# Kernel tuning notes

Hardware: AMD Instinct MI355X
Metric: run time of the kernel (lower is better)

Reference implementation:

```python
import jax, jax.numpy as jnp
import numpy as np

EMBED_DIM = 512
NUM_HEADS = 8
HEAD_DIM = EMBED_DIM // NUM_HEADS
B, N, M = 4, 4096, 4096


def setup_inputs() -> dict:
    key = jax.random.key(0)
    ks = jax.random.split(key, 16)
    s = 0.02
    inp = {
        "query": jax.random.normal(ks[0], (B, N, EMBED_DIM), jnp.float32),
        "key": jax.random.normal(ks[1], (B, M, EMBED_DIM), jnp.float32),
        "value": jax.random.normal(ks[2], (B, M, EMBED_DIM), jnp.float32),
        # Linear weights stored as (in, out) so y = x @ W + b (== torch x @ W.T + b)
        "Wq": jax.random.normal(ks[3], (EMBED_DIM, EMBED_DIM), jnp.float32) * s,
        "bq": jnp.zeros((EMBED_DIM,), jnp.float32),
        "Wk": jax.random.normal(ks[4], (EMBED_DIM, EMBED_DIM), jnp.float32) * s,
        "bk": jnp.zeros((EMBED_DIM,), jnp.float32),
        "Wv": jax.random.normal(ks[5], (EMBED_DIM, EMBED_DIM), jnp.float32) * s,
        "bv": jnp.zeros((EMBED_DIM,), jnp.float32),
        # rank expansion MLP acts per-head on head_dim
        "W1": jax.random.normal(ks[6], (HEAD_DIM, HEAD_DIM * 2), jnp.float32) * s,
        "b1": jnp.zeros((HEAD_DIM * 2,), jnp.float32),
        "W2": jax.random.normal(ks[7], (HEAD_DIM * 2, HEAD_DIM), jnp.float32) * s,
        "b2": jnp.zeros((HEAD_DIM,), jnp.float32),
        "Wo": jax.random.normal(ks[8], (EMBED_DIM, EMBED_DIM), jnp.float32) * s,
        "bo": jnp.zeros((EMBED_DIM,), jnp.float32),
    }
    return inp


def reference(query, key, value, Wq, bq, Wk, bk, Wv, bv, W1, b1, W2, b2, Wo, bo):
    b, n, _ = query.shape
    m = key.shape[1]
    H, D = NUM_HEADS, HEAD_DIM
    # ELU+1 feature maps on projected q, k
    q = jax.nn.elu(query @ Wq + bq) + 1.0           # [B,N,E]
    k = jax.nn.elu(key @ Wk + bk) + 1.0             # [B,M,E]
    v = value @ Wv + bv                              # [B,M,E]
    q = q.reshape(b, n, H, D)
    k = k.reshape(b, m, H, D)
    v = v.reshape(b, m, H, D)
    # rank expansion MLP on keys (per head_dim), exact GELU as nn.GELU default
    k_aug = jax.nn.gelu(k @ W1 + b1, approximate=False) @ W2 + b2
    k_aug = jax.nn.elu(k_aug) + 1.0                  # [B,M,H,D]
    # inputs already fp32 (torch .float() casts are identity here)
    k_scaled = k_aug / m                             # normalize over context len
    kv_context = jnp.einsum('bmhd,bmhe->bhde', k_scaled, v)   # [B,H,D,D]
    out = jnp.einsum('bnhd,bhde->bnhe', q, kv_context)        # [B,N,H,D]
    k_sum = k_scaled.sum(axis=1)                      # [B,H,D]
    denom = jnp.einsum('bnhd,bhd->bnh', q, k_sum)     # [B,N,H]
    out = out / jnp.clip(denom, 1e-6, None)[..., None]
    out = jnp.clip(jnp.nan_to_num(out, nan=0.0, posinf=65000.0, neginf=-65000.0),
                   -65000.0, 65000.0)
    out = out.reshape(b, n, H * D)
    return out @ Wo + bo
```

## Files before the change

kernel.cpp:

```cpp
#include <hip/hip_runtime.h>
#include <hip/hip_bf16.h>
#include <cmath>

#define DEV __device__ __forceinline__

typedef __bf16 bf16x8 __attribute__((ext_vector_type(8)));
typedef float f32x4 __attribute__((ext_vector_type(4)));
typedef unsigned int u32;
typedef unsigned short u16;

#define S_VMCNT(N) asm volatile("s_waitcnt vmcnt(" #N ")" ::: "memory")
#define S_LGKM0    asm volatile("s_waitcnt lgkmcnt(0)" ::: "memory")
#define S_FENCE    asm volatile("" ::: "memory")
#define S_BAR      __builtin_amdgcn_s_barrier()

DEV u16 f2bf(float f) {
  union { float f; u32 u; } v;
  v.f = f;
  u32 u = v.u;
  u += 0x7fffu + ((u >> 16) & 1u);
  return (u16)(u >> 16);
}
DEV u32 pk2(float a, float b) {
  union { __hip_bfloat162 h2; u32 u; } v;
  v.h2 = __float22bfloat162_rn(float2{a, b});
  return v.u;
}

DEV void async16(const void* g, void* l) {
  __builtin_amdgcn_global_load_lds((const __attribute__((address_space(1))) u32*)g,
                                   (__attribute__((address_space(3))) u32*)l, 16, 0, 0);
}

DEV int swz(int row, int kq) { return row * 64 + ((kq * 8) ^ ((row & 7) << 3)); }

struct PArgs {
  const float* wsrc[6];
  u16* wdst[6];
  int K[6];
  int N[6];
  const float* xsrc[3];
  u16* xdst[3];
};
__global__ __launch_bounds__(256)
void prep_all(PArgs a)
{
  __shared__ u16 t[64][72];
  const int tid = threadIdx.x;

  if (blockIdx.y == 3) {
    const int x = blockIdx.x;
    const int m = x >> 6;
    const int kt = ((x >> 3) & 7) * 64, nt = (x & 7) * 64;
    const int K = a.K[m], N = a.N[m];
    if (kt >= K || nt >= N) return;
    const float* src = a.wsrc[m];
    u16* dst = a.wdst[m];
    const int tx = tid & 15, ty = tid >> 4;
#pragma unroll
    for (int rr = 0; rr < 64; rr += 16) {
      const int k = kt + ty + rr;
      float4 v = *(const float4*)(src + (long)k * N + nt + tx * 4);
      t[tx * 4 + 0][ty + rr] = f2bf(v.x);
      t[tx * 4 + 1][ty + rr] = f2bf(v.y);
      t[tx * 4 + 2][ty + rr] = f2bf(v.z);
      t[tx * 4 + 3][ty + rr] = f2bf(v.w);
    }
    __syncthreads();
    if (m < 4) {
      const int ktile = kt >> 6;
#pragma unroll
      for (int it = 0; it < 2; ++it) {
        const int s = tid + it * 256;
        const int r = s >> 3, c = (s & 7) * 8;
        const int n = nt + r;
        const int colblk = n >> 7, cl = n & 127;
        ushort4 u0 = *(ushort4*)&t[r][c];
        ushort4 u1 = *(ushort4*)&t[r][c + 4];
        u16* d = dst + ((long)colblk * 8 + ktile) * 8192 + cl * 64 + (c ^ ((cl & 7) << 3));
        *(ushort4*)d = u0;
        *(ushort4*)(d + 4) = u1;
      }
    } else {
#pragma unroll
      for (int it = 0; it < 2; ++it) {
        const int s = tid + it * 256;
        const int r = s >> 3, c = (s & 7) * 8;
        ushort4 u0 = *(ushort4*)&t[r][c];
        ushort4 u1 = *(ushort4*)&t[r][c + 4];
        *(ushort4*)(dst + (long)(nt + r) * K + kt + c) = u0;
        *(ushort4*)(dst + (long)(nt + r) * K + kt + c + 4) = u1;
      }
    }
  } else {
    if (blockIdx.x >= 256) return;
    const int z = blockIdx.y;
    const float* src = a.xsrc[z];
    u16* dst = a.xdst[z];
    const long r0 = (long)blockIdx.x * 64;
    const int wv = tid >> 6, lane = tid & 63;
    const int row_lo = lane >> 3, kq = lane & 7;
#pragma unroll 4
    for (int it = 0; it < 16; ++it) {
      const int c = it * 4 + wv;
      const int kt = c & 7, row_hi = c >> 3;
      const int row = row_hi * 8 + row_lo;
      const long ng = r0 + row;
      const int rb = (int)(ng >> 7), rl = (int)(ng & 127);
      const float* s = src + ng * 512 + kt * 64 + kq * 8;
      float4 lo = *(const float4*)s, hi = *(const float4*)(s + 4);
      union { u32 q[4]; uint4 v; } pk;
      pk.q[0] = pk2(lo.x, lo.y); pk.q[1] = pk2(lo.z, lo.w);
      pk.q[2] = pk2(hi.x, hi.y); pk.q[3] = pk2(hi.z, hi.w);
      *(uint4*)(dst + ((long)rb * 8 + kt) * 8192 + rl * 64 + ((kq * 8) ^ ((rl & 7) << 3))) = pk.v;
    }
  }
}

__global__ __launch_bounds__(256, 2)
void qkv_gemm(const u16* __restrict__ qbI, const u16* __restrict__ kbI,
              const u16* __restrict__ vbI, const u16* __restrict__ WqP,
              const u16* __restrict__ WkP, const u16* __restrict__ WvP,
              const float* __restrict__ bq, const float* __restrict__ bk,
              const float* __restrict__ bv, const u16* __restrict__ W1T,
              const u16* __restrict__ W2T, const float* __restrict__ b1,
              const float* __restrict__ b2, u16* __restrict__ qact,
              u16* __restrict__ vT, u16* __restrict__ kaT, float invM)
{
  __shared__ __align__(16) u16 SB[32768];

  const int z = blockIdx.z;
  const u16* Ai = z == 0 ? qbI : z == 1 ? kbI : vbI;
  const u16* Bp = z == 0 ? WqP : z == 1 ? WkP : WvP;
  const float* bias = z == 0 ? bq : z == 1 ? bk : bv;

  const int tid = threadIdx.x, wv = tid >> 6, lane = tid & 63;
  const int wr = wv >> 1, wc = wv & 1;
  const int lrow = lane & 15, lq = lane >> 4;
  const long r0 = (long)blockIdx.x * 128;
  const int c0 = blockIdx.y * 128;

  auto stage = [&](int T, u16* buf) {
#pragma unroll
    for (int it = 0; it < 4; ++it) {
      const int sl = it * 256 + wv * 64;
      async16(Ai + ((long)blockIdx.x * 8 + T) * 8192 + (sl + lane) * 8, &buf[sl * 8]);
      async16(Bp + ((long)blockIdx.y * 8 + T) * 8192 + (sl + lane) * 8, &buf[8192 + sl * 8]);
    }
  };

  f32x4 acc[4][4] = {};
  stage(0, SB);
  S_VMCNT(0);
  S_BAR;

#pragma unroll
  for (int t = 0; t < 8; ++t) {
    const int cur = t & 1, nxt = 1 - cur;
    if (t < 7) stage(t + 1, SB + nxt * 16384);
    const u16* Ac = SB + cur * 16384;
    const u16* Bc = Ac + 8192;
#pragma unroll
    for (int subk = 0; subk < 2; ++subk) {
      bf16x8 af[4], bfr[4];
#pragma unroll
      for (int i = 0; i < 4; ++i)
        af[i] = *(const bf16x8*)&Ac[swz(wr * 64 + i * 16 + lrow, subk * 4 + lq)];
#pragma unroll
      for (int j = 0; j < 4; ++j)
        bfr[j] = *(const bf16x8*)&Bc[swz(wc * 64 + j * 16 + lrow, subk * 4 + lq)];
#pragma unroll
      for (int i = 0; i < 4; ++i)
#pragma unroll
        for (int j = 0; j < 4; ++j)
          acc[i][j] = __builtin_amdgcn_mfma_f32_16x16x32_bf16(af[i], bfr[j], acc[i][j], 0, 0, 0);
    }
    S_LGKM0;
    if (t < 7) { S_VMCNT(0); }
    S_BAR;
  }

  if (z == 0) {
    u16* LTq = SB + wv * 4608;
#pragma unroll
    for (int i = 0; i < 4; ++i) {
#pragma unroll
      for (int j = 0; j < 4; ++j) {
        const int col = c0 + wc * 64 + j * 16 + lrow;
        const float bvv = bias[col];
        const int cloc = j * 16 + lrow;
#pragma unroll
        for (int p = 0; p < 4; ++p) {
          float o = acc[i][j][p] + bvv;
          o = (o > 0.f) ? (o + 1.f) : __expf(o);
          LTq[(i * 16 + lq * 4 + p) * 72 + cloc] = f2bf(o);
        }
      }
    }
    __syncthreads();
#pragma unroll
    for (int ps = 0; ps < 8; ++ps) {
      const int rloc = ps * 8 + (lane >> 3);
      const int coff = (lane & 7) * 8;
      uint4 v = *(const uint4*)&LTq[rloc * 72 + coff];
      *(uint4*)(qact + (r0 + wr * 64 + rloc) * 512 + c0 + wc * 64 + coff) = v;
    }
  } else if (z == 2) {
    u16* LTv = SB + wv * 4608;
#pragma unroll
    for (int i = 0; i < 4; ++i) {
#pragma unroll
      for (int j = 0; j < 4; ++j) {
        const int col = c0 + wc * 64 + j * 16 + lrow;
        const float bvv = bias[col];
        ushort4 w;
        w.x = f2bf(acc[i][j][0] + bvv);
        w.y = f2bf(acc[i][j][1] + bvv);
        w.z = f2bf(acc[i][j][2] + bvv);
        w.w = f2bf(acc[i][j][3] + bvv);
        *(ushort4*)&LTv[(j * 16 + lrow) * 72 + i * 16 + lq * 4] = w;
      }
    }
    const int b = (int)(r0 >> 12);
    const int h = (c0 + wc * 64) >> 6;
    const int mg0 = (int)(r0 & 4095) + wr * 64;
    __syncthreads();
#pragma unroll
    for (int ps = 0; ps < 8; ++ps) {
      const int e = ps * 8 + (lane >> 3);
      const int mq = (lane & 7) * 8;
      uint4 v = *(const uint4*)&LTv[e * 72 + mq];
      *(uint4*)(vT + (((long)b * 8 + h) * 64 + e) * 4096 + mg0 + mq) = v;
    }
  } else {
    u16* As_k = SB;
    u16* hid  = SB + 16384;
    const int b   = (int)(r0 >> 12);
    const int m0g = (int)(r0 & 4095);
    const int h0  = c0 >> 6;

    __syncthreads();
#pragma unroll
    for (int i = 0; i < 4; ++i)
#pragma unroll
      for (int j = 0; j < 4; ++j) {
        const int col = c0 + wc * 64 + j * 16 + lrow;
        const float bvv = bias[col];
        const int d = j * 16 + lrow;
#pragma unroll
        for (int p = 0; p < 4; ++p) {
          const int m = wr * 64 + i * 16 + lq * 4 + p;
          float o = acc[i][j][p] + bvv;
          o = (o > 0.f) ? (o + 1.f) : __expf(o);
          As_k[wc * 8192 + m * 64 + ((((d >> 3) ^ (m & 7)) << 3) | (d & 7))] = f2bf(o);
        }
      }
    __syncthreads();

    const int c0m = (wv >> 1) * 64, mh0 = (wv & 1) * 64;
    const int d0  = (wv >> 1) * 32, mh2 = (wv & 1) * 64;

    for (int hh = 0; hh < 2; ++hh) {
      f32x4 acc1[4][4] = {};
#pragma unroll
      for (int kt = 0; kt < 2; ++kt) {
        bf16x8 wa[4], kb[4];
#pragma unroll
        for (int i = 0; i < 4; ++i)
          wa[i] = *(const bf16x8*)(W1T + (c0m + i * 16 + lrow) * 64 + kt * 32 + lq * 8);
#pragma unroll
        for (int j = 0; j < 4; ++j) {
          const int m = mh0 + j * 16 + lrow;
          kb[j] = *(const bf16x8*)&As_k[hh * 8192 + m * 64 + (((kt * 4 + lq) ^ (m & 7)) << 3)];
        }
#pragma unroll
        for (int i = 0; i < 4; ++i)
#pragma unroll
          for (int j = 0; j < 4; ++j)
            acc1[i][j] = __builtin_amdgcn_mfma_f32_16x16x32_bf16(wa[i], kb[j], acc1[i][j], 0, 0, 0);
      }

#pragma unroll
      for (int i = 0; i < 4; ++i) {
        const int cc = c0m + i * 16 + lq * 4;
        float4 bv4 = *(const float4*)(b1 + cc);
#pragma unroll
        for (int j = 0; j < 4; ++j) {
          const int m = mh0 + j * 16 + lrow;
          float x0 = acc1[i][j][0] + bv4.x, x1 = acc1[i][j][1] + bv4.y;
          float x2 = acc1[i][j][2] + bv4.z, x3 = acc1[i][j][3] + bv4.w;
          ushort4 w;
          w.x = f2bf(0.5f * x0 * (1.f + erff(x0 * 0.7071067811865475f)));
          w.y = f2bf(0.5f * x1 * (1.f + erff(x1 * 0.7071067811865475f)));
          w.z = f2bf(0.5f * x2 * (1.f + erff(x2 * 0.7071067811865475f)));
          w.w = f2bf(0.5f * x3 * (1.f + erff(x3 * 0.7071067811865475f)));
          *(ushort4*)&hid[m * 128 + ((((cc >> 3) ^ (m & 7)) << 3) | (cc & 7))] = w;
        }
      }
      __syncthreads();

      f32x4 acc2[4][2] = {};
#pragma unroll
      for (int kt = 0; kt < 4; ++kt) {
        bf16x8 wa2[2], hb[4];
#pragma unroll
        for (int i = 0; i < 2; ++i)
          wa2[i] = *(const bf16x8*)(W2T + (d0 + i * 16 + lrow) * 128 + kt * 32 + lq * 8);
#pragma unroll
        for (int j = 0; j < 4; ++j) {
          const int m = mh2 + j * 16 + lrow;
          hb[j] = *(const bf16x8*)&hid[m * 128 + (((kt * 4 + lq) ^ (m & 7)) << 3)];
        }
#pragma unroll
        for (int j = 0; j < 4; ++j)
#pragma unroll
          for (int i = 0; i < 2; ++i)
            acc2[j][i] = __builtin_amdgcn_mfma_f32_16x16x32_bf16(hb[j], wa2[i], acc2[j][i], 0, 0, 0);
      }

      u16* LT2 = SB + hh * 8192;
#pragma unroll
      for (int i = 0; i < 2; ++i) {
        const int d = d0 + i * 16 + lrow;
        const float bd = b2[d];
#pragma unroll
        for (int j = 0; j < 4; ++j) {
          const int ml = mh2 + j * 16 + lq * 4;
          ushort4 w;
#pragma unroll
          for (int p = 0; p < 4; ++p) {
            float v = acc2[j][i][p] + bd;
            v = ((v > 0.f) ? (v + 1.f) : __expf(v)) * invM;
            ((u16*)&w)[p] = f2bf(v);
          }
          *(ushort4*)&LT2[d * 128 + ((((ml >> 3) ^ (d & 7)) << 3) | (ml & 7))] = w;
        }
      }
      __syncthreads();

      const int bh2 = b * 8 + h0 + hh;
#pragma unroll
      for (int it = 0; it < 4; ++it) {
        const int u = it * 256 + tid;
        const int mo = u & 15, hd = u >> 4;
        uint4 v = *(const uint4*)&LT2[hd * 128 + ((mo ^ (hd & 7)) << 3)];
        *(uint4*)(kaT + ((long)bh2 * 64 + hd) * 4096 + m0g + mo * 8) = v;
      }
    }
  }
}

__global__ __launch_bounds__(256, 2)
void out_gemm(const u16* __restrict__ A, const u16* __restrict__ Bt,
              const float* __restrict__ bias, float* __restrict__ Y)
{
  __shared__ __align__(16) u16 SB[32768];
  const int tid = threadIdx.x, wv = tid >> 6, lane = tid & 63;
  const int wr = wv >> 1, wc = wv & 1;
  const int lrow = lane & 15, lq = lane >> 4;
  const long r0 = (long)blockIdx.x * 128;
  const int c0 = blockIdx.y * 128;

  auto stage = [&](int T, u16* buf) {
#pragma unroll
    for (int it = 0; it < 4; ++it) {
      const int sl = it * 256 + wv * 64;
      async16(A  + ((long)blockIdx.x * 8 + T) * 8192 + (sl + lane) * 8, &buf[sl * 8]);
      async16(Bt + ((long)blockIdx.y * 8 + T) * 8192 + (sl + lane) * 8, &buf[8192 + sl * 8]);
    }
  };

  f32x4 acc[4][4] = {};
  stage(0, SB);
  S_VMCNT(0);
  S_BAR;

#pragma unroll
  for (int t = 0; t < 8; ++t) {
    const int cur = t & 1, nxt = 1 - cur;
    if (t < 7) stage(t + 1, SB + nxt * 16384);
    const u16* Ac = SB + cur * 16384;
    const u16* Bc = Ac + 8192;
#pragma unroll
    for (int subk = 0; subk < 2; ++subk) {
      bf16x8 af[4], bfr[4];
#pragma unroll
      for (int i = 0; i < 4; ++i)
        af[i] = *(const bf16x8*)&Ac[swz(wr * 64 + i * 16 + lrow, subk * 4 + lq)];
#pragma unroll
      for (int j = 0; j < 4; ++j)
        bfr[j] = *(const bf16x8*)&Bc[swz(wc * 64 + j * 16 + lrow, subk * 4 + lq)];
#pragma unroll
      for (int i = 0; i < 4; ++i)
#pragma unroll
        for (int j = 0; j < 4; ++j)
          acc[i][j] = __builtin_amdgcn_mfma_f32_16x16x32_bf16(af[i], bfr[j], acc[i][j], 0, 0, 0);
    }
    S_LGKM0;
    if (t < 7) { S_VMCNT(0); }
    S_BAR;
  }
#pragma unroll
  for (int i = 0; i < 4; ++i) {
#pragma unroll
    for (int j = 0; j < 4; ++j) {
      const int col = c0 + wc * 64 + j * 16 + lrow;
      const float bv = bias[col];
#pragma unroll
      for (int p = 0; p < 4; ++p) {
        const long row = r0 + wr * 64 + i * 16 + lq * 4 + p;
        Y[row * 512 + col] = acc[i][j][p] + bv;
      }
    }
  }
}

__global__ __launch_bounds__(256, 2)
void kv_gemm(const u16* __restrict__ kaT, const u16* __restrict__ vT,
             float* __restrict__ kvp, float* __restrict__ ksp)
{
  const int sp = blockIdx.x;
  const int bh = blockIdx.y;
  __shared__ __align__(16) u16 SB[32768];
  const int tid = threadIdx.x, wv = tid >> 6, lane = tid & 63;
  const int lrow = lane & 15, lq = lane >> 4;
  f32x4 acc[4][4] = {};
  f32x4 accs[4] = {};
  bf16x8 ones;
#pragma unroll
  for (int z = 0; z < 8; ++z) ones[z] = (__bf16)1.0f;
  const long base = (long)bh * 64 * 4096;

#pragma unroll
  for (int ph = 0; ph < 2; ++ph) {
    const int m0 = sp * 256 + ph * 128;
#pragma unroll
    for (int i = 0; i < 4; ++i) {
      const int s = (wv * 4 + i) * 64 + lane;
      const int chunk = s >> 8, row = (s >> 2) & 63, part = s & 3;
      const long g = base + (long)row * 4096 + m0 + chunk * 32 + part * 8;
      async16(kaT + g, &SB[ph * 16384 + (wv * 4 + i) * 512]);
      async16(vT + g, &SB[ph * 16384 + 8192 + (wv * 4 + i) * 512]);
    }
    S_FENCE;
  }

#pragma unroll
  for (int ph = 0; ph < 2; ++ph) {
    if (ph == 0) { S_VMCNT(8); } else { S_VMCNT(0); }
    const u16* As = SB + ph * 16384;
    const u16* Bs = As + 8192;
    bf16x8 af[4], bfr[4];
#pragma unroll
    for (int i = 0; i < 4; ++i)
      af[i] = *(const bf16x8*)&As[wv * 2048 + (i * 16 + lrow) * 32 + lq * 8];
#pragma unroll
    for (int j = 0; j < 4; ++j)
      bfr[j] = *(const bf16x8*)&Bs[wv * 2048 + (j * 16 + lrow) * 32 + lq * 8];
#pragma unroll
    for (int i = 0; i < 4; ++i) {
#pragma unroll
      for (int j = 0; j < 4; ++j)
        acc[i][j] = __builtin_amdgcn_mfma_f32_16x16x32_bf16(af[i], bfr[j], acc[i][j], 0, 0, 0);
      accs[i] = __builtin_amdgcn_mfma_f32_16x16x32_bf16(af[i], ones, accs[i], 0, 0, 0);
    }
  }

  float* red = (float*)SB;
  float* ksr = red + 64 * 68;
  for (int w = 0; w < 4; ++w) {
    __syncthreads();
    if (wv == w) {
#pragma unroll
      for (int i = 0; i < 4; ++i) {
#pragma unroll
        for (int j = 0; j < 4; ++j) {
          const int e = j * 16 + lrow, dd = i * 16 + lq * 4;
          float* p = &red[e * 68 + dd];
          if (w == 0) { p[0] = acc[i][j][0]; p[1] = acc[i][j][1]; p[2] = acc[i][j][2]; p[3] = acc[i][j][3]; }
          else        { p[0] += acc[i][j][0]; p[1] += acc[i][j][1]; p[2] += acc[i][j][2]; p[3] += acc[i][j][3]; }
        }
        if (lrow == 0) {
          const int dd = i * 16 + lq * 4;
#pragma unroll
          for (int p2 = 0; p2 < 4; ++p2) {
            if (w == 0) ksr[dd + p2] = accs[i][p2];
            else        ksr[dd + p2] += accs[i][p2];
          }
        }
      }
    }
  }
  __syncthreads();
  float* kvo = kvp + ((long)sp * 32 + bh) * 4096;
  for (int s = tid; s < 4096; s += 256) kvo[s] = red[(s >> 6) * 68 + (s & 63)];
  if (tid < 64) ksp[(sp * 32 + bh) * 64 + tid] = ksr[tid];
}

__global__ __launch_bounds__(256)
void kv_reduce(const float* __restrict__ kvp, const float* __restrict__ ksp,
               u16* __restrict__ kvT, u16* __restrict__ ksumT)
{
  const int bh = blockIdx.x;
  const int t = threadIdx.x;
  const int s0 = blockIdx.y * 512;
#pragma unroll
  for (int i = 0; i < 2; ++i) {
    const int s = s0 + i * 256 + t;
    float v = 0.f;
#pragma unroll
    for (int sp = 0; sp < 16; ++sp) v += kvp[((long)sp * 32 + bh) * 4096 + s];
    kvT[(long)bh * 4096 + s] = f2bf(v);
  }
  if (blockIdx.y == 0 && t < 64) {
    float v = 0.f;
#pragma unroll
    for (int sp = 0; sp < 16; ++sp) v += ksp[(sp * 32 + bh) * 64 + t];
    ksumT[bh * 64 + t] = f2bf(v);
  }
}

__global__ __launch_bounds__(256)
void attn_mfma(const u16* __restrict__ q, const u16* __restrict__ kvT,
               const u16* __restrict__ ksumT, u16* __restrict__ attn)
{
  __shared__ u16 SB[17408];
  const int tid = threadIdx.x, wv = tid >> 6, lane = tid & 63;
  const int lrow = lane & 15, lq = lane >> 4;
  const int n0 = blockIdx.x * 256;
  const int bh = blockIdx.y, b = bh >> 3, h = bh & 7;
  u16* As = SB;

#pragma unroll
  for (int half = 0; half < 2; ++half)
#pragma unroll
    for (int i = 0; i < 4; ++i) {
      const int s = (wv * 4 + i) * 64 + lane;
      async16(q + ((long)(b * 4096 + n0 + (s >> 2))) * 512 + h * 64 + half * 32 + (s & 3) * 8,
              &As[half * 8192 + (wv * 4 + i) * 512]);
    }
  bf16x8 bfr[2][4], ks[2];
#pragma unroll
  for (int half = 0; half < 2; ++half) {
#pragma unroll
    for (int j = 0; j < 4; ++j)
      bfr[half][j] = *(const bf16x8*)(kvT + ((long)bh * 64 + j * 16 + lrow) * 64 + half * 32 + lq * 8);
    ks[half] = *(const bf16x8*)(ksumT + bh * 64 + half * 32 + lq * 8);
  }
  __syncthreads();

  f32x4 acc[4][4] = {};
  f32x4 accd[4] = {};
#pragma unroll
  for (int half = 0; half < 2; ++half) {
    bf16x8 af[4];
#pragma unroll
    for (int i = 0; i < 4; ++i)
      af[i] = *(const bf16x8*)&As[half * 8192 + (wv * 64 + i * 16 + lrow) * 32 + lq * 8];
#pragma unroll
    for (int i = 0; i < 4; ++i) {
#pragma unroll
      for (int j = 0; j < 4; ++j)
        acc[i][j] = __builtin_amdgcn_mfma_f32_16x16x32_bf16(af[i], bfr[half][j], acc[i][j], 0, 0, 0);
      accd[i] = __builtin_amdgcn_mfma_f32_16x16x32_bf16(af[i], ks[half], accd[i], 0, 0, 0);
    }
  }
  __syncthreads();

  u16* LT = SB;
#pragma unroll
  for (int i = 0; i < 4; ++i) {
    float dinv[4];
#pragma unroll
    for (int p = 0; p < 4; ++p) dinv[p] = 1.f / fmaxf(accd[i][p], 1e-6f);
#pragma unroll
    for (int j = 0; j < 4; ++j) {
      const int e = j * 16 + lrow;
      const int nl0 = i * 16 + lq * 4;
      ushort4 w;
      float x0 = acc[i][j][0] * dinv[0], x1 = acc[i][j][1] * dinv[1];
      float x2 = acc[i][j][2] * dinv[2], x3 = acc[i][j][3] * dinv[3];
      if (!(x0 == x0)) x0 = 0.f;
      if (!(x1 == x1)) x1 = 0.f;
      if (!(x2 == x2)) x2 = 0.f;
      if (!(x3 == x3)) x3 = 0.f;
      w.x = f2bf(fminf(65000.f, fmaxf(-65000.f, x0)));
      w.y = f2bf(fminf(65000.f, fmaxf(-65000.f, x1)));
      w.z = f2bf(fminf(65000.f, fmaxf(-65000.f, x2)));
      w.w = f2bf(fminf(65000.f, fmaxf(-65000.f, x3)));
      *(ushort4*)&LT[wv * 4352 + e * 68 + nl0] = w;
    }
  }
  __syncthreads();
#pragma unroll
  for (int it = 0; it < 8; ++it) {
    const int c = it * 256 + tid;
    const int n = c & 255, ec = c >> 8;
    const int wr2 = n >> 6, nl = n & 63;
    ushort4 w0, w1;
    w0.x = LT[wr2 * 4352 + (ec * 8 + 0) * 68 + nl];
    w0.y = LT[wr2 * 4352 + (ec * 8 + 1) * 68 + nl];
    w0.z = LT[wr2 * 4352 + (ec * 8 + 2) * 68 + nl];
    w0.w = LT[wr2 * 4352 + (ec * 8 + 3) * 68 + nl];
    w1.x = LT[wr2 * 4352 + (ec * 8 + 4) * 68 + nl];
    w1.y = LT[wr2 * 4352 + (ec * 8 + 5) * 68 + nl];
    w1.z = LT[wr2 * 4352 + (ec * 8 + 6) * 68 + nl];
    w1.w = LT[wr2 * 4352 + (ec * 8 + 7) * 68 + nl];
    const int ng = b * 4096 + n0 + n;
    const int rowblk = ng >> 7, rl = ng & 127;
    u16* dst = attn + ((long)rowblk * 8 + h) * 8192 + rl * 64 + ((ec * 8) ^ ((rl & 7) << 3));
    *(ushort4*)dst = w0;
    *(ushort4*)(dst + 4) = w1;
  }
}

static constexpr long U = 8388608;

extern "C" void kernel_launch(void* const* d_in, const int* in_sizes, int n_in,
                              void* d_out, int out_size, void* d_ws, size_t ws_size,
                              hipStream_t stream)
{
  const float* query = (const float*)d_in[0];
  const float* key   = (const float*)d_in[1];
  const float* value = (const float*)d_in[2];
  const float* Wq = (const float*)d_in[3];
  const float* bq = (const float*)d_in[4];
  const float* Wk = (const float*)d_in[5];
  const float* bk = (const float*)d_in[6];
  const float* Wv = (const float*)d_in[7];
  const float* bv = (const float*)d_in[8];
  const float* W1 = (const float*)d_in[9];
  const float* b1 = (const float*)d_in[10];
  const float* W2 = (const float*)d_in[11];
  const float* b2 = (const float*)d_in[12];
  const float* Wo = (const float*)d_in[13];
  const float* bo = (const float*)d_in[14];

  u16* wsh = (u16*)d_ws;
  u16* qact = wsh;
  u16* qb   = wsh + U;
  u16* vT   = wsh + 2 * U;
  u16* kaT  = wsh + 3 * U;
  u16* attn = wsh + 4 * U;
  u16* vb   = wsh + 4 * U;
  u16* kb   = (u16*)d_out;

  float* fp  = (float*)(wsh + 5 * U);
  float* kvp = fp;
  float* ksp = fp + 2097152;
  u16* kvTg   = (u16*)(fp + 2129920);
  u16* ksumTg = kvTg + 131072;
  u16* wtb = ksumTg + 2048;
  u16* WqT = wtb;
  u16* WkT = wtb + 262144;
  u16* WvT = wtb + 524288;
  u16* WoT = wtb + 786432;
  u16* W1T = wtb + 1048576;
  u16* W2T = wtb + 1056768;

  dim3 blk(256);
  const float invM = 1.f / 4096.f;

  PArgs pa;
  pa.wsrc[0] = Wq; pa.wdst[0] = WqT; pa.K[0] = 512; pa.N[0] = 512;
  pa.wsrc[1] = Wk; pa.wdst[1] = WkT; pa.K[1] = 512; pa.N[1] = 512;
  pa.wsrc[2] = Wv; pa.wdst[2] = WvT; pa.K[2] = 512; pa.N[2] = 512;
  pa.wsrc[3] = Wo; pa.wdst[3] = WoT; pa.K[3] = 512; pa.N[3] = 512;
  pa.wsrc[4] = W1; pa.wdst[4] = W1T; pa.K[4] = 64;  pa.N[4] = 128;
  pa.wsrc[5] = W2; pa.wdst[5] = W2T; pa.K[5] = 128; pa.N[5] = 64;
  pa.xsrc[0] = query; pa.xdst[0] = qb;
  pa.xsrc[1] = key;   pa.xdst[1] = kb;
  pa.xsrc[2] = value; pa.xdst[2] = vb;
  prep_all<<<dim3(384, 4), blk, 0, stream>>>(pa);

  qkv_gemm<<<dim3(128, 4, 3), blk, 0, stream>>>(qb, kb, vb, WqT, WkT, WvT,
                                                bq, bk, bv, W1T, W2T, b1, b2,
                                                qact, vT, kaT, invM);
  kv_gemm<<<dim3(16, 32), blk, 0, stream>>>(kaT, vT, kvp, ksp);
  kv_reduce<<<dim3(32, 8), blk, 0, stream>>>(kvp, ksp, kvTg, ksumTg);
  attn_mfma<<<dim3(16, 32), blk, 0, stream>>>(qact, kvTg, ksumTg, attn);
  out_gemm<<<dim3(128, 4), blk, 0, stream>>>(attn, WoT, bo, (float*)d_out);
}
```

Before: 257.0 us.

## Fuse attention normalization into output projection GEMM, dropping attn buffer

Replaces the separate attention kernel and output GEMM with one kernel. For each 128-row tile it loops over heads: it computes q·kv and the denominator with MFMA, normalizes and clamps, writes the bf16 tile to shared memory, then multiplies it by the matching Wo slice. This removes a global intermediate round trip and a launch. In exchange, the q·kv work is repeated for each of the 4 output column blocks, and each head iteration adds extra barriers and scalar LDS stores.

```diff
diff --git a/kernel.cpp b/kernel.cpp
--- a/kernel.cpp
+++ b/kernel.cpp
@@ -351,71 +351,6 @@
 }
 
 __global__ __launch_bounds__(256, 2)
-void out_gemm(const u16* __restrict__ A, const u16* __restrict__ Bt,
-              const float* __restrict__ bias, float* __restrict__ Y)
-{
-  __shared__ __align__(16) u16 SB[32768];
-  const int tid = threadIdx.x, wv = tid >> 6, lane = tid & 63;
-  const int wr = wv >> 1, wc = wv & 1;
-  const int lrow = lane & 15, lq = lane >> 4;
-  const long r0 = (long)blockIdx.x * 128;
-  const int c0 = blockIdx.y * 128;
-
-  auto stage = [&](int T, u16* buf) {
-#pragma unroll
-    for (int it = 0; it < 4; ++it) {
-      const int sl = it * 256 + wv * 64;
-      async16(A  + ((long)blockIdx.x * 8 + T) * 8192 + (sl + lane) * 8, &buf[sl * 8]);
-      async16(Bt + ((long)blockIdx.y * 8 + T) * 8192 + (sl + lane) * 8, &buf[8192 + sl * 8]);
-    }
-  };
-
-  f32x4 acc[4][4] = {};
-  stage(0, SB);
-  S_VMCNT(0);
-  S_BAR;
-
-#pragma unroll
-  for (int t = 0; t < 8; ++t) {
-    const int cur = t & 1, nxt = 1 - cur;
-    if (t < 7) stage(t + 1, SB + nxt * 16384);
-    const u16* Ac = SB + cur * 16384;
-    const u16* Bc = Ac + 8192;
-#pragma unroll
-    for (int subk = 0; subk < 2; ++subk) {
-      bf16x8 af[4], bfr[4];
-#pragma unroll
-      for (int i = 0; i < 4; ++i)
-        af[i] = *(const bf16x8*)&Ac[swz(wr * 64 + i * 16 + lrow, subk * 4 + lq)];
-#pragma unroll
-      for (int j = 0; j < 4; ++j)
-        bfr[j] = *(const bf16x8*)&Bc[swz(wc * 64 + j * 16 + lrow, subk * 4 + lq)];
-#pragma unroll
-      for (int i = 0; i < 4; ++i)
-#pragma unroll
-        for (int j = 0; j < 4; ++j)
-          acc[i][j] = __builtin_amdgcn_mfma_f32_16x16x32_bf16(af[i], bfr[j], acc[i][j], 0, 0, 0);
-    }
-    S_LGKM0;
-    if (t < 7) { S_VMCNT(0); }
-    S_BAR;
-  }
-#pragma unroll
-  for (int i = 0; i < 4; ++i) {
-#pragma unroll
-    for (int j = 0; j < 4; ++j) {
-      const int col = c0 + wc * 64 + j * 16 + lrow;
-      const float bv = bias[col];
-#pragma unroll
-      for (int p = 0; p < 4; ++p) {
-        const long row = r0 + wr * 64 + i * 16 + lq * 4 + p;
-        Y[row * 512 + col] = acc[i][j][p] + bv;
-      }
-    }
-  }
-}
-
-__global__ __launch_bounds__(256, 2)
 void kv_gemm(const u16* __restrict__ kaT, const u16* __restrict__ vT,
              float* __restrict__ kvp, float* __restrict__ ksp)
 {
@@ -520,97 +455,135 @@
   }
 }
 
-__global__ __launch_bounds__(256)
-void attn_mfma(const u16* __restrict__ q, const u16* __restrict__ kvT,
-               const u16* __restrict__ ksumT, u16* __restrict__ attn)
+__global__ __launch_bounds__(256, 2)
+void attn_out(const u16* __restrict__ qact, const u16* __restrict__ kvT,
+              const u16* __restrict__ ksumT, const u16* __restrict__ WoP,
+              const float* __restrict__ bias, float* __restrict__ Y)
 {
-  __shared__ u16 SB[17408];
+  __shared__ __align__(16) u16 SB[32768];
   const int tid = threadIdx.x, wv = tid >> 6, lane = tid & 63;
+  const int wr = wv >> 1, wc = wv & 1;
   const int lrow = lane & 15, lq = lane >> 4;
-  const int n0 = blockIdx.x * 256;
-  const int bh = blockIdx.y, b = bh >> 3, h = bh & 7;
-  u16* As = SB;
-
-#pragma unroll
-  for (int half = 0; half < 2; ++half)
+  const long r0 = (long)blockIdx.x * 128;
+  const int c0 = blockIdx.y * 128;
+  const int b = (int)(r0 >> 12);
+
+  auto stageQ = [&](int h, u16* buf) {
+#pragma unroll
+    for (int it = 0; it < 4; ++it) {
+      const int s = it * 256 + wv * 64 + lane;
+      const int row = s >> 3, p = s & 7;
+      const int kq = p ^ (row & 7);
+      async16(qact + (r0 + row) * 512 + h * 64 + kq * 8, &buf[(it * 256 + wv * 64) * 8]);
+    }
+  };
+  auto stageW = [&](int h, u16* buf) {
+#pragma unroll
+    for (int it = 0; it < 4; ++it) {
+      const int sl = it * 256 + wv * 64;
+      async16(WoP + ((long)blockIdx.y * 8 + h) * 8192 + (sl + lane) * 8, &buf[sl * 8]);
+    }
+  };
+
+  f32x4 accO[4][4] = {};
+  stageQ(0, SB);
+  stageW(0, SB + 16384);
+  __syncthreads();
+
+  for (int h = 0; h < 8; ++h) {
+    const int cur = h & 1, nxt = 1 - cur;
+    u16* Qc = SB + cur * 8192;
+    u16* Wc = SB + 16384 + cur * 8192;
+    const int bh = b * 8 + h;
+
+    bf16x8 kvf[2][2], ks[2];
+#pragma unroll
+    for (int sk = 0; sk < 2; ++sk) {
+#pragma unroll
+      for (int j = 0; j < 2; ++j)
+        kvf[sk][j] = *(const bf16x8*)(kvT + (long)bh * 4096 +
+                       (wc * 32 + j * 16 + lrow) * 64 + sk * 32 + lq * 8);
+      ks[sk] = *(const bf16x8*)(ksumT + bh * 64 + sk * 32 + lq * 8);
+    }
+
+    f32x4 accS[4][2] = {};
+    f32x4 accD[4] = {};
+#pragma unroll
+    for (int sk = 0; sk < 2; ++sk) {
+      bf16x8 af[4];
+#pragma unroll
+      for (int i = 0; i < 4; ++i)
+        af[i] = *(const bf16x8*)&Qc[swz(wr * 64 + i * 16 + lrow, sk * 4 + lq)];
+#pragma unroll
+      for (int i = 0; i < 4; ++i) {
+#pragma unroll
+        for (int j = 0; j < 2; ++j)
+          accS[i][j] = __builtin_amdgcn_mfma_f32_16x16x32_bf16(af[i], kvf[sk][j], accS[i][j], 0, 0, 0);
+        accD[i] = __builtin_amdgcn_mfma_f32_16x16x32_bf16(af[i], ks[sk], accD[i], 0, 0, 0);
+      }
+    }
+    __syncthreads();
+
+    if (h < 7) { stageQ(h + 1, SB + nxt * 8192); stageW(h + 1, SB + 16384 + nxt * 8192); }
+
 #pragma unroll
     for (int i = 0; i < 4; ++i) {
-      const int s = (wv * 4 + i) * 64 + lane;
-      async16(q + ((long)(b * 4096 + n0 + (s >> 2))) * 512 + h * 64 + half * 32 + (s & 3) * 8,
-              &As[half * 8192 + (wv * 4 + i) * 512]);
-    }
-  bf16x8 bfr[2][4], ks[2];
-#pragma unroll
-  for (int half = 0; half < 2; ++half) {
-#pragma unroll
-    for (int j = 0; j < 4; ++j)
-      bfr[half][j] = *(const bf16x8*)(kvT + ((long)bh * 64 + j * 16 + lrow) * 64 + half * 32 + lq * 8);
-    ks[half] = *(const bf16x8*)(ksumT + bh * 64 + half * 32 + lq * 8);
-  }
-  __syncthreads();
-
-  f32x4 acc[4][4] = {};
-  f32x4 accd[4] = {};
-#pragma unroll
-  for (int half = 0; half < 2; ++half) {
-    bf16x8 af[4];
-#pragma unroll
-    for (int i = 0; i < 4; ++i)
-      af[i] = *(const bf16x8*)&As[half * 8192 + (wv * 64 + i * 16 + lrow) * 32 + lq * 8];
-#pragma unroll
-    for (int i = 0; i < 4; ++i) {
+      float dinv[4];
+#pragma unroll
+      for (int p = 0; p < 4; ++p) dinv[p] = 1.f / fmaxf(accD[i][p], 1e-6f);
+#pragma unroll
+      for (int j = 0; j < 2; ++j) {
+        const int e = wc * 32 + j * 16 + lrow;
+        float x0 = accS[i][j][0] * dinv[0], x1 = accS[i][j][1] * dinv[1];
+        float x2 = accS[i][j][2] * dinv[2], x3 = accS[i][j][3] * dinv[3];
+        if (!(x0 == x0)) x0 = 0.f;
+        if (!(x1 == x1)) x1 = 0.f;
+        if (!(x2 == x2)) x2 = 0.f;
+        if (!(x3 == x3)) x3 = 0.f;
+        u16 w0 = f2bf(fminf(65000.f, fmaxf(-65000.f, x0)));
+        u16 w1 = f2bf(fminf(65000.f, fmaxf(-65000.f, x1)));
+        u16 w2 = f2bf(fminf(65000.f, fmaxf(-65000.f, x2)));
+        u16 w3 = f2bf(fminf(65000.f, fmaxf(-65000.f, x3)));
+#pragma unroll
+        for (int p = 0; p < 4; ++p) {
+          const int row = wr * 64 + i * 16 + lq * 4 + p;
+          const u16 wval = p == 0 ? w0 : p == 1 ? w1 : p == 2 ? w2 : w3;
+          Qc[row * 64 + ((((e >> 3) ^ (row & 7)) << 3) | (e & 7))] = wval;
+        }
+      }
+    }
+    __syncthreads();
+
+#pragma unroll
+    for (int sk = 0; sk < 2; ++sk) {
+      bf16x8 ap[4], bw[4];
+#pragma unroll
+      for (int i = 0; i < 4; ++i)
+        ap[i] = *(const bf16x8*)&Qc[swz(wr * 64 + i * 16 + lrow, sk * 4 + lq)];
 #pragma unroll
       for (int j = 0; j < 4; ++j)
-        acc[i][j] = __builtin_amdgcn_mfma_f32_16x16x32_bf16(af[i], bfr[half][j], acc[i][j], 0, 0, 0);
-      accd[i] = __builtin_amdgcn_mfma_f32_16x16x32_bf16(af[i], ks[half], accd[i], 0, 0, 0);
-    }
-  }
-  __syncthreads();
-
-  u16* LT = SB;
+        bw[j] = *(const bf16x8*)&Wc[swz(wc * 64 + j * 16 + lrow, sk * 4 + lq)];
+#pragma unroll
+      for (int i = 0; i < 4; ++i)
+#pragma unroll
+        for (int j = 0; j < 4; ++j)
+          accO[i][j] = __builtin_amdgcn_mfma_f32_16x16x32_bf16(ap[i], bw[j], accO[i][j], 0, 0, 0);
+    }
+    __syncthreads();
+  }
+
 #pragma unroll
   for (int i = 0; i < 4; ++i) {
-    float dinv[4];
-#pragma unroll
-    for (int p = 0; p < 4; ++p) dinv[p] = 1.f / fmaxf(accd[i][p], 1e-6f);
 #pragma unroll
     for (int j = 0; j < 4; ++j) {
-      const int e = j * 16 + lrow;
-      const int nl0 = i * 16 + lq * 4;
-      ushort4 w;
-      float x0 = acc[i][j][0] * dinv[0], x1 = acc[i][j][1] * dinv[1];
-      float x2 = acc[i][j][2] * dinv[2], x3 = acc[i][j][3] * dinv[3];
-      if (!(x0 == x0)) x0 = 0.f;
-      if (!(x1 == x1)) x1 = 0.f;
-      if (!(x2 == x2)) x2 = 0.f;
-      if (!(x3 == x3)) x3 = 0.f;
-      w.x = f2bf(fminf(65000.f, fmaxf(-65000.f, x0)));
-      w.y = f2bf(fminf(65000.f, fmaxf(-65000.f, x1)));
-      w.z = f2bf(fminf(65000.f, fmaxf(-65000.f, x2)));
-      w.w = f2bf(fminf(65000.f, fmaxf(-65000.f, x3)));
-      *(ushort4*)&LT[wv * 4352 + e * 68 + nl0] = w;
-    }
-  }
-  __syncthreads();
-#pragma unroll
-  for (int it = 0; it < 8; ++it) {
-    const int c = it * 256 + tid;
-    const int n = c & 255, ec = c >> 8;
-    const int wr2 = n >> 6, nl = n & 63;
-    ushort4 w0, w1;
-    w0.x = LT[wr2 * 4352 + (ec * 8 + 0) * 68 + nl];
-    w0.y = LT[wr2 * 4352 + (ec * 8 + 1) * 68 + nl];
-    w0.z = LT[wr2 * 4352 + (ec * 8 + 2) * 68 + nl];
-    w0.w = LT[wr2 * 4352 + (ec * 8 + 3) * 68 + nl];
-    w1.x = LT[wr2 * 4352 + (ec * 8 + 4) * 68 + nl];
-    w1.y = LT[wr2 * 4352 + (ec * 8 + 5) * 68 + nl];
-    w1.z = LT[wr2 * 4352 + (ec * 8 + 6) * 68 + nl];
-    w1.w = LT[wr2 * 4352 + (ec * 8 + 7) * 68 + nl];
-    const int ng = b * 4096 + n0 + n;
-    const int rowblk = ng >> 7, rl = ng & 127;
-    u16* dst = attn + ((long)rowblk * 8 + h) * 8192 + rl * 64 + ((ec * 8) ^ ((rl & 7) << 3));
-    *(ushort4*)dst = w0;
-    *(ushort4*)(dst + 4) = w1;
+      const int col = c0 + wc * 64 + j * 16 + lrow;
+      const float bv = bias[col];
+#pragma unroll
+      for (int p = 0; p < 4; ++p) {
+        const long row = r0 + wr * 64 + i * 16 + lq * 4 + p;
+        Y[row * 512 + col] = accO[i][j][p] + bv;
+      }
+    }
   }
 }
 
@@ -641,7 +614,6 @@
   u16* qb   = wsh + U;
   u16* vT   = wsh + 2 * U;
   u16* kaT  = wsh + 3 * U;
-  u16* attn = wsh + 4 * U;
   u16* vb   = wsh + 4 * U;
   u16* kb   = (u16*)d_out;
 
@@ -678,6 +650,6 @@
                                                 qact, vT, kaT, invM);
   kv_gemm<<<dim3(16, 32), blk, 0, stream>>>(kaT, vT, kvp, ksp);
   kv_reduce<<<dim3(32, 8), blk, 0, stream>>>(kvp, ksp, kvTg, ksumTg);
-  attn_mfma<<<dim3(16, 32), blk, 0, stream>>>(qact, kvTg, ksumTg, attn);
-  out_gemm<<<dim3(128, 4), blk, 0, stream>>>(attn, WoT, bo, (float*)d_out);
-}
+  attn_out<<<dim3(128, 4), blk, 0, stream>>>(qact, kvTg, ksumTg, WoT, bo,
+                                             (float*)d_out);
+}
```

After: 274.6 us. 6.9% more time.
